# Optimization experiments

Measured on AMD Instinct MI355X. Metric: run time of the kernel, lower is better.

Reference implementation:

```python
import jax, jax.numpy as jnp
import numpy as np

# dims
T, N, F, B = 8, 100000, 128, 4096        # snapshots, graph nodes, in_features, seed batch
S1, S2 = 5, 2                             # sampling fanouts (sizes=[5,2])
H1, H2, O, C = 512, 64, 32, 2             # hids=[512,64], out_features, nchannels
TIME_MOD = 2
W_POS, W_NOPOS = 0.6, 0.4
V_TH = 1.0                                # invth=1


@jax.custom_vjp
def spike(v):
    # IF/LIF firing with threshold V_TH (spikingjelly-style heaviside)
    return (v >= V_TH).astype(v.dtype)

def _spike_fwd(v):
    return spike(v), v

def _spike_bwd(v, g):
    # triangle surrogate gradient, alpha=1.0
    return (g * jnp.maximum(0.0, 1.0 - jnp.abs(v - V_TH)),)

spike.defvjp(_spike_fwd, _spike_bwd)


def sinusoid_table(n_pos, d):
    # vectorized port of get_sinusoid_encoding_table
    pos = np.arange(n_pos, dtype=np.float32)[:, None]
    i = np.arange(d)[None, :]
    angle = pos / (10000.0 ** (2.0 * (i // 2) / d))
    tab = np.where(i % 2 == 0, np.sin(angle), np.cos(angle)).astype(np.float32)
    return jnp.asarray(tab)


def srga_single(h0, h1, h2, Ws1, Wn1, Ws2, Wn2):
    """2-layer sampled-SAGE with spiking activations (one snapshot).
    h0:[B,F] seeds, h1:[B*S1,F] hop1, h2:[B*S1*S2,F] hop2."""
    n0, n1 = h0.shape[0], h1.shape[0]
    # layer 1 applied at levels 0 and 1 (mean neighbor aggregation, no bias)
    agg0 = h1.reshape(n0, S1, -1).mean(axis=1)
    s0 = spike(h0 @ Ws1 + agg0 @ Wn1)            # [B, H1]
    agg1 = h2.reshape(n1, S2, -1).mean(axis=1)
    s1 = spike(h1 @ Ws1 + agg1 @ Wn1)            # [B*S1, H1]
    # layer 2 fuses level-1 spikes into seeds
    agg = s1.reshape(n0, S1, -1).mean(axis=1)
    return spike(s0 @ Ws2 + agg @ Wn2)            # [B, H2]


def temporal_attn(seq, w, b, pos):
    # seq: [T', B, H2]; matches TemporalAttention (softmax over time)
    if pos is not None:
        seq = seq + pos[:seq.shape[0], None, :]
    scores = jnp.einsum('tbh,ho->tbo', seq, w) + b       # [T',B,1]
    wts = jax.nn.softmax(scores, axis=0)[..., 0]          # [T',B]
    return jnp.einsum('tbh,tb->bh', seq, wts)             # [B,H2]


def setup_inputs():
    key = jax.random.key(0)
    ks = jax.random.split(key, 14)
    nodes = jax.random.randint(ks[0], (B,), 0, N)
    hop1_idx = jax.random.randint(ks[1], (T, B * S1), 0, N)
    hop2_idx = jax.random.randint(ks[2], (T, B * S1 * S2), 0, N)
    x = jax.random.normal(ks[3], (T, N, F), dtype=jnp.float32)
    inp = {
        'nodes': nodes, 'hop1_idx': hop1_idx, 'hop2_idx': hop2_idx, 'x': x,
        'Wself1': jax.random.normal(ks[4], (C, F, H1), jnp.float32) / np.sqrt(F).astype(np.float32),
        'Wnbr1': jax.random.normal(ks[5], (C, F, H1), jnp.float32) / np.sqrt(F).astype(np.float32),
        'Wself2': jax.random.normal(ks[6], (C, H1, H2), jnp.float32) / np.sqrt(H1).astype(np.float32),
        'Wnbr2': jax.random.normal(ks[7], (C, H1, H2), jnp.float32) / np.sqrt(H1).astype(np.float32),
        'attn_pos_w': jax.random.normal(ks[8], (C, H2, 1), jnp.float32) / np.sqrt(H2).astype(np.float32),
        'attn_pos_b': jax.random.normal(ks[9], (C, 1), jnp.float32) * 0.01,
        'attn_nopos_w': jax.random.normal(ks[10], (C, H2, 1), jnp.float32) / np.sqrt(H2).astype(np.float32),
        'attn_nopos_b': jax.random.normal(ks[11], (C, 1), jnp.float32) * 0.01,
        'mtg_w': jax.random.normal(ks[12], (H2, O), jnp.float32) / np.sqrt(H2).astype(np.float32),
        'mtg_b': jax.random.normal(ks[13], (O,), jnp.float32) * 0.01,
    }
    return inp


def reference(nodes, hop1_idx, hop2_idx, x, Wself1, Wnbr1, Wself2, Wnbr2,
              attn_pos_w, attn_pos_b, attn_nopos_w, attn_nopos_b, mtg_w, mtg_b):
    tidx = jnp.arange(T)
    # irregular gathers per snapshot (the memory-bound hot path)
    h0 = x[tidx[:, None], nodes[None, :]]     # [T, B, F]
    h1 = x[tidx[:, None], hop1_idx]           # [T, B*S1, F]
    h2 = x[tidx[:, None], hop2_idx]           # [T, B*S1*S2, F]
    pos_tab = sinusoid_table(T, H2)
    channel_embs = []
    for c in range(C):
        if c == 0:
            hs = (h0, h1, h2)                 # channel 0: every step
        else:
            hs = (h0[::TIME_MOD], h1[::TIME_MOD], h2[::TIME_MOD])  # channel 1: t % time_mod == 0
        outs = jax.vmap(
            lambda a, b_, d_, c=c: srga_single(a, b_, d_, Wself1[c], Wnbr1[c], Wself2[c], Wnbr2[c])
        )(*hs)                                # [T', B, H2]
        emb_pos = temporal_attn(outs, attn_pos_w[c], attn_pos_b[c], pos_tab)
        emb_nopos = temporal_attn(outs, attn_nopos_w[c], attn_nopos_b[c], None)
        channel_embs.append(W_POS * emb_pos + W_NOPOS * emb_nopos)
    stacked = jnp.stack(channel_embs, axis=0).mean(axis=0)  # [B, H2]
    return stacked @ mtg_w + mtg_b                          # [B, O]
```

## Files before the change

### kernel.cpp

```cpp
#include <hip/hip_runtime.h>
#include <math.h>

typedef _Float16 f16;
typedef _Float16 f16x8 __attribute__((ext_vector_type(8)));
typedef float f32x4 __attribute__((ext_vector_type(4)));

#define T_ 8
#define NNODES 100000
#define F_ 128
#define B_ 4096
#define S1_ 5
#define S2_ 2
#define H1_ 512
#define H2_ 64
#define O_ 32
#define M1 (B_ + B_*S1_)
#define K1 (2*F_)
#define NZ 12

__device__ __forceinline__ float wsum64(float v) {
#pragma unroll
  for (int o = 32; o > 0; o >>= 1) v += __shfl_xor(v, o, 64);
  return v;
}

__global__ __launch_bounds__(512) void postab_kernel(float* __restrict__ postab) {
  int i = threadIdx.x;
  int p = i >> 6, d = i & 63;
  double ang = (double)p / pow(10000.0, (2.0 * (double)(d >> 1)) / 64.0);
  postab[i] = (float)((d & 1) ? cos(ang) : sin(ang));
}

__global__ __launch_bounds__(256)
void prep_w(const float* __restrict__ Ws1, const float* __restrict__ Wn1,
            f16* __restrict__ Bth, f16* __restrict__ Btl) {
  const int bid = blockIdx.x;
  const int c = bid >> 9, n = bid & 511;
  const int k = threadIdx.x;
  float wv = (k < F_) ? Ws1[((size_t)c * F_ + k) * H1_ + n]
                      : Wn1[((size_t)c * F_ + (k - F_)) * H1_ + n];
  f16 hi = (f16)wv;
  f16 lo = (f16)((wv - (float)hi) * 2048.0f);
  size_t o = ((size_t)c * H1_ + n) * K1 + k;
  Bth[o] = hi; Btl[o] = lo;
}

__global__ __launch_bounds__(256)
void prep_w2(const float* __restrict__ Ws2, const float* __restrict__ Wn2,
             f16* __restrict__ B2h, f16* __restrict__ B2l) {
  const int c = blockIdx.x >> 6, n = blockIdx.x & 63;
#pragma unroll
  for (int q = 0; q < 4; ++q) {
    const int k = q * 256 + threadIdx.x;
    float v = (k < H1_) ? Ws2[((size_t)c * H1_ + k) * H2_ + n]
                        : 0.2f * Wn2[((size_t)c * H1_ + (k - H1_)) * H2_ + n];
    f16 hi = (f16)v;
    f16 lo = (f16)((v - (float)hi) * 2048.0f);
    size_t o = ((size_t)c * H2_ + n) * 1024 + k;
    B2h[o] = hi; B2l[o] = lo;
  }
}

__global__ __launch_bounds__(256) void gather_kernel(
    const int* __restrict__ nodes, const int* __restrict__ hop1,
    const int* __restrict__ hop2, const float* __restrict__ x,
    f16* __restrict__ Ah, f16* __restrict__ Al)
{
  const int t = blockIdx.y;
  const int r = blockIdx.x * 4 + (threadIdx.x >> 6);
  const int lane = threadIdx.x & 63;
  const int fo = (lane & 31) << 2;
  const bool hpart = lane < 32;
  const float* xt = x + (size_t)t * NNODES * F_;
  float4 v;
  if (r < B_) {
    if (hpart) {
      v = *(const float4*)(xt + (size_t)nodes[r] * F_ + fo);
    } else {
      v = make_float4(0.f, 0.f, 0.f, 0.f);
#pragma unroll
      for (int s = 0; s < S1_; ++s) {
        int idx = hop1[t * (B_ * S1_) + r * S1_ + s];
        float4 u = *(const float4*)(xt + (size_t)idx * F_ + fo);
        v.x += u.x; v.y += u.y; v.z += u.z; v.w += u.w;
      }
      v.x /= 5.0f; v.y /= 5.0f; v.z /= 5.0f; v.w /= 5.0f;
    }
  } else {
    const int j = r - B_;
    if (hpart) {
      v = *(const float4*)(xt + (size_t)hop1[t * (B_ * S1_) + j] * F_ + fo);
    } else {
      v = make_float4(0.f, 0.f, 0.f, 0.f);
#pragma unroll
      for (int s = 0; s < S2_; ++s) {
        int idx = hop2[t * (B_ * S1_ * S2_) + j * S2_ + s];
        float4 u = *(const float4*)(xt + (size_t)idx * F_ + fo);
        v.x += u.x; v.y += u.y; v.z += u.z; v.w += u.w;
      }
      v.x *= 0.5f; v.y *= 0.5f; v.z *= 0.5f; v.w *= 0.5f;
    }
  }
  union { f16 h[4]; uint2 u; } H, L;
  float vv[4] = {v.x, v.y, v.z, v.w};
#pragma unroll
  for (int e = 0; e < 4; ++e) {
    f16 hi = (f16)vv[e];
    H.h[e] = hi;
    L.h[e] = (f16)((vv[e] - (float)hi) * 2048.0f);
  }
  const size_t base = ((size_t)t * M1 + r) * K1 + 4 * lane;
  *(uint2*)(Ah + base) = H.u;
  *(uint2*)(Al + base) = L.u;
}

__global__ __launch_bounds__(512)
void gemm1_mfma(const f16* __restrict__ Ah, const f16* __restrict__ Al,
                const f16* __restrict__ Bth, const f16* __restrict__ Btl,
                unsigned char* __restrict__ Sbase)
{
  const int hid = blockIdx.x + 4 * blockIdx.y + 384 * blockIdx.z;
  const int xcd = hid & 7, ii = hid >> 3;
  const int nblk = ii & 3;
  const int pair = xcd * 144 + (ii >> 2);
  const int yblk = pair % 96;
  const int z    = pair / 96;

  const int t = (z < 8) ? z : 2 * (z - 8);
  const int c = (z < 8) ? 0 : 1;
  const int m0 = yblk * 256;
  const int n0 = nblk * 128;
  const int tid = threadIdx.x;
  const int lane = tid & 63;
  const int w = tid >> 6;
  const int wr = w >> 1, wc = w & 1;

  __shared__ f16 lds[3][24576];

  const f16* tbAh = Ah  + (size_t)t * M1 * K1;
  const f16* tbAl = Al  + (size_t)t * M1 * K1;
  const f16* tbBh = Bth + (size_t)c * H1_ * K1;
  const f16* tbBl = Btl + (size_t)c * H1_ * K1;

  const f16* srcp[6];
#pragma unroll
  for (int q = 0; q < 6; ++q) {
    const int u = q * 512 + tid;
    const f16* base; int row, grow;
    if (u < 1024)      { base = tbAh; row = u >> 2;          grow = m0 + row; }
    else if (u < 2048) { base = tbAl; row = (u - 1024) >> 2; grow = m0 + row; }
    else if (u < 2560) { base = tbBh; row = (u - 2048) >> 2; grow = n0 + row; }
    else               { base = tbBl; row = (u - 2560) >> 2; grow = n0 + row; }
    const int kc = (u & 3) ^ (row & 3);
    srcp[q] = base + (size_t)grow * K1 + kc * 8;
  }

  auto stage = [&](int buf) {
#pragma unroll
    for (int q = 0; q < 6; ++q) {
      __builtin_amdgcn_global_load_lds(
          (const __attribute__((address_space(1))) void*)srcp[q],
          (__attribute__((address_space(3))) void*)((char*)lds + buf * 49152 + (q * 8 + w) * 1024),
          16, 0, 0);
      srcp[q] += 32;
    }
  };

  f32x4 accm[4][4], accc[4][4];
#pragma unroll
  for (int i = 0; i < 4; ++i)
#pragma unroll
    for (int j = 0; j < 4; ++j) {
      accm[i][j] = (f32x4){0.f, 0.f, 0.f, 0.f};
      accc[i][j] = (f32x4){0.f, 0.f, 0.f, 0.f};
    }

  const int kg = lane >> 4;
  const int lr = lane & 15;
  const int ks = (kg ^ (lr & 3)) * 8;

  stage(0);
  stage(1);
  __syncthreads();

#pragma unroll
  for (int kt = 0; kt < 8; ++kt) {
    const int cur = kt % 3;
    const f16* bufp = &lds[cur][0];

    f16x8 ah[4], bh[4];
#pragma unroll
    for (int i = 0; i < 4; ++i) ah[i] = *(const f16x8*)(bufp + (wr * 64 + i * 16 + lr) * 32 + ks);
#pragma unroll
    for (int j = 0; j < 4; ++j) bh[j] = *(const f16x8*)(bufp + 16384 + (wc * 64 + j * 16 + lr) * 32 + ks);
    if (kt < 6) stage((kt + 2) % 3);
    __builtin_amdgcn_s_setprio(1);
#pragma unroll
    for (int j = 0; j < 4; ++j)
#pragma unroll
      for (int i = 0; i < 4; ++i)
        accm[i][j] = __builtin_amdgcn_mfma_f32_16x16x32_f16(ah[i], bh[j], accm[i][j], 0, 0, 0);
    __builtin_amdgcn_s_setprio(0);

    f16x8 bl[4];
#pragma unroll
    for (int j = 0; j < 4; ++j) bl[j] = *(const f16x8*)(bufp + 20480 + (wc * 64 + j * 16 + lr) * 32 + ks);
    __builtin_amdgcn_s_setprio(1);
#pragma unroll
    for (int j = 0; j < 4; ++j)
#pragma unroll
      for (int i = 0; i < 4; ++i)
        accc[i][j] = __builtin_amdgcn_mfma_f32_16x16x32_f16(ah[i], bl[j], accc[i][j], 0, 0, 0);
    __builtin_amdgcn_s_setprio(0);

    f16x8 al[4];
#pragma unroll
    for (int i = 0; i < 4; ++i) al[i] = *(const f16x8*)(bufp + 8192 + (wr * 64 + i * 16 + lr) * 32 + ks);
    __builtin_amdgcn_s_setprio(1);
#pragma unroll
    for (int j = 0; j < 4; ++j)
#pragma unroll
      for (int i = 0; i < 4; ++i)
        accc[i][j] = __builtin_amdgcn_mfma_f32_16x16x32_f16(al[i], bh[j], accc[i][j], 0, 0, 0);
    __builtin_amdgcn_s_setprio(0);

    if (kt == 1 || kt == 3 || kt == 5) {
      __syncthreads();
    } else if (kt == 0 || kt == 2 || kt == 4) {
      asm volatile("s_waitcnt lgkmcnt(0)" ::: "memory");
      __builtin_amdgcn_s_barrier();
      __builtin_amdgcn_sched_barrier(0);
    }
  }

  unsigned char* S = Sbase + (size_t)z * M1 * H1_;
#pragma unroll
  for (int i = 0; i < 4; ++i)
#pragma unroll
    for (int j = 0; j < 4; ++j) {
      const int n = n0 + wc * 64 + j * 16 + lr;
#pragma unroll
      for (int r = 0; r < 4; ++r) {
        const int m = m0 + wr * 64 + i * 16 + kg * 4 + r;
        float v = accm[i][j][r] + accc[i][j][r] * 4.8828125e-4f;
        S[(size_t)m * H1_ + n] = (v >= 1.0f) ? 1 : 0;
      }
    }
}

__global__ __launch_bounds__(256)
void gemm2_fused(const unsigned char* __restrict__ Sbase,
                 const f16* __restrict__ B2h, const f16* __restrict__ B2l,
                 unsigned char* __restrict__ outsbase)
{
  const int z = blockIdx.y;
  const int c = (z < 8) ? 0 : 1;
  const int m0 = blockIdx.x * 128;
  const int tid = threadIdx.x;
  const int lane = tid & 63;
  const int wv = tid >> 6;

  __shared__ f16 lds2[2][8192];

  const unsigned char* Sz = Sbase + (size_t)z * M1 * H1_;
  const f16* Bhc = B2h + (size_t)c * H2_ * 1024;
  const f16* Blc = B2l + (size_t)c * H2_ * 1024;

  const f16* srcB[2];
#pragma unroll
  for (int q = 0; q < 2; ++q) {
    const int v = q * 256 + tid;
    if (v < 256) {
      const int k8 = v >> 6, row = v & 63;
      srcB[q] = Bhc + (size_t)row * 1024 + k8 * 8;
    } else {
      const int v2 = v - 256, k8 = v2 >> 6, row = v2 & 63;
      srcB[q] = Blc + (size_t)row * 1024 + k8 * 8;
    }
  }
  auto stageB = [&](int buf) {
#pragma unroll
    for (int q = 0; q < 2; ++q) {
      __builtin_amdgcn_global_load_lds(
          (const __attribute__((address_space(1))) void*)srcB[q],
          (__attribute__((address_space(3))) void*)((char*)lds2 + buf * 16384 + 8192 + q * 4096 + wv * 1024),
          16, 0, 0);
      srcB[q] += 32;
    }
  };

  const int arow = tid >> 1;
  const int ahalf = tid & 1;
  const int k8b = ahalf * 2;

  auto loadS = [&](int kt, uint4* regs) {
    if (kt < 16) {
      regs[0] = *(const uint4*)(Sz + (size_t)(m0 + arow) * H1_ + kt * 32 + ahalf * 16);
    } else {
      const int k0 = (kt - 16) * 32 + ahalf * 16;
#pragma unroll
      for (int s = 0; s < S1_; ++s)
        regs[s] = *(const uint4*)(Sz + ((size_t)B_ + (size_t)(m0 + arow) * S1_ + s) * H1_ + k0);
    }
  };
  auto writeA = [&](int buf, int kt, const uint4* regs) {
    uint4 b;
    if (kt < 16) {
      b = regs[0];
    } else {
      b.x = regs[0].x + regs[1].x + regs[2].x + regs[3].x + regs[4].x;
      b.y = regs[0].y + regs[1].y + regs[2].y + regs[3].y + regs[4].y;
      b.z = regs[0].z + regs[1].z + regs[2].z + regs[3].z + regs[4].z;
      b.w = regs[0].w + regs[1].w + regs[2].w + regs[3].w + regs[4].w;
    }
    union { uint4 v; unsigned char by[16]; } U; U.v = b;
    union { f16 h[8]; uint4 v; } P0, P1;
#pragma unroll
    for (int e = 0; e < 8; ++e) {
      P0.h[e] = (f16)(int)U.by[e];
      P1.h[e] = (f16)(int)U.by[8 + e];
    }
    f16* dst = &lds2[buf][0];
    *(uint4*)(dst + ((size_t)k8b * 128 + arow) * 8)       = P0.v;
    *(uint4*)(dst + ((size_t)(k8b + 1) * 128 + arow) * 8) = P1.v;
  };

  f32x4 acch[2][4], accl[2][4];
#pragma unroll
  for (int i = 0; i < 2; ++i)
#pragma unroll
    for (int j = 0; j < 4; ++j) {
      acch[i][j] = (f32x4){0.f, 0.f, 0.f, 0.f};
      accl[i][j] = (f32x4){0.f, 0.f, 0.f, 0.f};
    }

  const int kg = lane >> 4;
  const int lr = lane & 15;

  {
    uint4 regs[5];
    loadS(0, regs);
    stageB(0);
    writeA(0, 0, regs);
  }
  __syncthreads();

#pragma unroll 1
  for (int kt = 0; kt < 32; ++kt) {
    const int cur = kt & 1;
    uint4 regs[5];
    if (kt < 31) {
      stageB(cur ^ 1);
      loadS(kt + 1, regs);
    }

    f16x8 a[2];
#pragma unroll
    for (int i = 0; i < 2; ++i)
      a[i] = *(const f16x8*)&lds2[cur][(size_t)(kg * 128 + wv * 32 + i * 16 + lr) * 8];
#pragma unroll
    for (int j = 0; j < 4; ++j) {
      f16x8 bh = *(const f16x8*)&lds2[cur][4096 + (size_t)(kg * 64 + j * 16 + lr) * 8];
      f16x8 bl = *(const f16x8*)&lds2[cur][6144 + (size_t)(kg * 64 + j * 16 + lr) * 8];
#pragma unroll
      for (int i = 0; i < 2; ++i) {
        acch[i][j] = __builtin_amdgcn_mfma_f32_16x16x32_f16(a[i], bh, acch[i][j], 0, 0, 0);
        accl[i][j] = __builtin_amdgcn_mfma_f32_16x16x32_f16(a[i], bl, accl[i][j], 0, 0, 0);
      }
    }
    if (kt < 31) writeA(cur ^ 1, kt + 1, regs);
    __syncthreads();
  }

  unsigned char* outs = outsbase + (size_t)z * B_ * H2_;
#pragma unroll
  for (int i = 0; i < 2; ++i)
#pragma unroll
    for (int j = 0; j < 4; ++j) {
      const int n = j * 16 + lr;
#pragma unroll
      for (int r = 0; r < 4; ++r) {
        const int m = m0 + wv * 32 + i * 16 + kg * 4 + r;
        float v = acch[i][j][r] + accl[i][j][r] * 4.8828125e-4f;
        outs[(size_t)m * H2_ + n] = (v >= 1.0f) ? 1 : 0;
      }
    }
}

__global__ __launch_bounds__(256)
void final_kernel(const unsigned char* __restrict__ outsbase,
                  const float* __restrict__ postab,
                  const float* __restrict__ apw, const float* __restrict__ apb,
                  const float* __restrict__ anw, const float* __restrict__ anb,
                  const float* __restrict__ mtgw, const float* __restrict__ mtgb,
                  float* __restrict__ out)
{
  const int b = blockIdx.x * 4 + (threadIdx.x >> 6);
  const int lane = threadIdx.x & 63;
  float stacked = 0.f;
#pragma unroll
  for (int c = 0; c < 2; ++c) {
    const int Tc = c ? 4 : 8;
    const int zb = c ? 8 : 0;
    const float wp = apw[c * H2_ + lane];
    const float wn = anw[c * H2_ + lane];
    float seqv[8], sp[8], sn[8];
#pragma unroll
    for (int tt = 0; tt < Tc; ++tt) {
      const float sv = (float)outsbase[((size_t)(zb + tt) * B_ + b) * H2_ + lane];
      seqv[tt] = sv;
      sp[tt] = wsum64((sv + postab[tt * H2_ + lane]) * wp);
      sn[tt] = wsum64(sv * wn);
    }
    const float bp = apb[c], bn = anb[c];
    float mp = -3.4e38f, mn = -3.4e38f;
#pragma unroll
    for (int tt = 0; tt < Tc; ++tt) {
      sp[tt] += bp; sn[tt] += bn;
      mp = fmaxf(mp, sp[tt]); mn = fmaxf(mn, sn[tt]);
    }
    float ep[8], en[8], sump = 0.f, sumn = 0.f;
#pragma unroll
    for (int tt = 0; tt < Tc; ++tt) {
      ep[tt] = expf(sp[tt] - mp);
      en[tt] = expf(sn[tt] - mn);
      sump += ep[tt]; sumn += en[tt];
    }
    float embp = 0.f, embn = 0.f;
#pragma unroll
    for (int tt = 0; tt < Tc; ++tt) {
      embp += (seqv[tt] + postab[tt * H2_ + lane]) * (ep[tt] / sump);
      embn += seqv[tt] * (en[tt] / sumn);
    }
    stacked += 0.5f * (0.6f * embp + 0.4f * embn);
  }
  float res = 0.f;
#pragma unroll
  for (int o = 0; o < O_; ++o) {
    float r = wsum64(stacked * mtgw[lane * O_ + o]);
    if (lane == o) res = r;
  }
  if (lane < O_) out[(size_t)b * O_ + lane] = res + mtgb[lane];
}

extern "C" void kernel_launch(void* const* d_in, const int* in_sizes, int n_in,
                              void* d_out, int out_size, void* d_ws, size_t ws_size,
                              hipStream_t stream)
{
  const int*   nodes  = (const int*)d_in[0];
  const int*   hop1   = (const int*)d_in[1];
  const int*   hop2   = (const int*)d_in[2];
  const float* x      = (const float*)d_in[3];
  const float* Wself1 = (const float*)d_in[4];
  const float* Wnbr1  = (const float*)d_in[5];
  const float* Wself2 = (const float*)d_in[6];
  const float* Wnbr2  = (const float*)d_in[7];
  const float* apw    = (const float*)d_in[8];
  const float* apb    = (const float*)d_in[9];
  const float* anw    = (const float*)d_in[10];
  const float* anb    = (const float*)d_in[11];
  const float* mtgw   = (const float*)d_in[12];
  const float* mtgb   = (const float*)d_in[13];
  float* out = (float*)d_out;

  char* ws = (char*)d_ws;
  size_t off = 0;
  float* postab = (float*)(ws + off);               off += 4096;
  f16* Ahb = (f16*)(ws + off);                      off += (size_t)T_ * M1 * K1 * 2;
  f16* Alb = (f16*)(ws + off);                      off += (size_t)T_ * M1 * K1 * 2;
  unsigned char* Sbase = (unsigned char*)(ws + off); off += (size_t)NZ * M1 * H1_;
  unsigned char* outsb = (unsigned char*)(ws + off); off += (size_t)NZ * B_ * H2_;
  if (ws_size < off) return;

  f16* Bth = (f16*)outsb;
  f16* Btl = Bth + (size_t)2 * H1_ * K1;
  f16* B2h = Alb;
  f16* B2l = B2h + (size_t)2 * H2_ * 1024;

  hipLaunchKernelGGL(postab_kernel, dim3(1), dim3(512), 0, stream, postab);
  hipLaunchKernelGGL(prep_w, dim3(1024), dim3(256), 0, stream, Wself1, Wnbr1, Bth, Btl);
  hipLaunchKernelGGL(gather_kernel, dim3(M1 / 4, T_), dim3(256), 0, stream,
                     nodes, hop1, hop2, x, Ahb, Alb);
  hipLaunchKernelGGL(gemm1_mfma, dim3(4, 96, NZ), dim3(512), 0, stream,
                     Ahb, Alb, Bth, Btl, Sbase);
  hipLaunchKernelGGL(prep_w2, dim3(128), dim3(256), 0, stream, Wself2, Wnbr2, B2h, B2l);
  hipLaunchKernelGGL(gemm2_fused, dim3(B_ / 128, NZ), dim3(256), 0, stream,
                     Sbase, B2h, B2l, outsb);
  hipLaunchKernelGGL(final_kernel, dim3(B_ / 4), dim3(256), 0, stream,
                     outsb, postab, apw, apb, anw, anb, mtgw, mtgb, out);
}
```

Before: 461.3 us.

## Load GEMM1 weight fragments directly from pre-laid-out global memory into registers

The weight matrix prep now writes the hi/lo fp16 weights in an MFMA-fragment-ordered layout, so each lane can read its 8-element B fragment with one vector load. GEMM1 stops staging B tiles through LDS and instead double-buffers B fragments in registers, prefetching the next k-step during the current one. This shrinks LDS per block from 144KB to 96KB and removes B-side LDS reads. In exchange it adds register pressure and relies on L2/cache hits for weight reads repeated across the two wave columns and many blocks.

```diff
diff --git a/kernel.cpp b/kernel.cpp
--- a/kernel.cpp
+++ b/kernel.cpp
@@ -41,7 +41,9 @@
                       : Wn1[((size_t)c * F_ + (k - F_)) * H1_ + n];
   f16 hi = (f16)wv;
   f16 lo = (f16)((wv - (float)hi) * 2048.0f);
-  size_t o = ((size_t)c * H1_ + n) * K1 + k;
+  const int ntile = n >> 4, lr = n & 15;
+  const int kt = k >> 5, kg = (k >> 3) & 3, ke = k & 7;
+  size_t o = ((((size_t)c * 32 + ntile) * 8 + kt) * 64 + kg * 16 + lr) * 8 + ke;
   Bth[o] = hi; Btl[o] = lo;
 }
 
@@ -129,42 +131,46 @@
   const int t = (z < 8) ? z : 2 * (z - 8);
   const int c = (z < 8) ? 0 : 1;
   const int m0 = yblk * 256;
-  const int n0 = nblk * 128;
   const int tid = threadIdx.x;
   const int lane = tid & 63;
   const int w = tid >> 6;
   const int wr = w >> 1, wc = w & 1;
 
-  __shared__ f16 lds[3][24576];
-
-  const f16* tbAh = Ah  + (size_t)t * M1 * K1;
-  const f16* tbAl = Al  + (size_t)t * M1 * K1;
-  const f16* tbBh = Bth + (size_t)c * H1_ * K1;
-  const f16* tbBl = Btl + (size_t)c * H1_ * K1;
-
-  const f16* srcp[6];
-#pragma unroll
-  for (int q = 0; q < 6; ++q) {
+  __shared__ f16 lds[3][16384];
+
+  const f16* tbAh = Ah + (size_t)t * M1 * K1;
+  const f16* tbAl = Al + (size_t)t * M1 * K1;
+
+  const f16* srcp[4];
+#pragma unroll
+  for (int q = 0; q < 4; ++q) {
     const int u = q * 512 + tid;
-    const f16* base; int row, grow;
-    if (u < 1024)      { base = tbAh; row = u >> 2;          grow = m0 + row; }
-    else if (u < 2048) { base = tbAl; row = (u - 1024) >> 2; grow = m0 + row; }
-    else if (u < 2560) { base = tbBh; row = (u - 2048) >> 2; grow = n0 + row; }
-    else               { base = tbBl; row = (u - 2560) >> 2; grow = n0 + row; }
+    const f16* base = (u < 1024) ? tbAh : tbAl;
+    const int row = (u & 1023) >> 2;
     const int kc = (u & 3) ^ (row & 3);
-    srcp[q] = base + (size_t)grow * K1 + kc * 8;
+    srcp[q] = base + (size_t)(m0 + row) * K1 + kc * 8;
   }
 
   auto stage = [&](int buf) {
 #pragma unroll
-    for (int q = 0; q < 6; ++q) {
+    for (int q = 0; q < 4; ++q) {
       __builtin_amdgcn_global_load_lds(
           (const __attribute__((address_space(1))) void*)srcp[q],
-          (__attribute__((address_space(3))) void*)((char*)lds + buf * 49152 + (q * 8 + w) * 1024),
+          (__attribute__((address_space(3))) void*)((char*)lds + buf * 32768 + (q * 8 + w) * 1024),
           16, 0, 0);
       srcp[q] += 32;
     }
   };
+
+  const f16* pBh[4];
+  const f16* pBl[4];
+#pragma unroll
+  for (int j = 0; j < 4; ++j) {
+    const int ntile = nblk * 8 + wc * 4 + j;
+    const size_t bo = (((size_t)c * 32 + ntile) * 8) * 512 + lane * 8;
+    pBh[j] = Bth + bo;
+    pBl[j] = Btl + bo;
+  }
 
   f32x4 accm[4][4], accc[4][4];
 #pragma unroll
@@ -179,6 +185,13 @@
   const int lr = lane & 15;
   const int ks = (kg ^ (lr & 3)) * 8;
 
+  f16x8 bH[2][4], bL[2][4];
+#pragma unroll
+  for (int j = 0; j < 4; ++j) {
+    bH[0][j] = *(const f16x8*)(pBh[j]);
+    bL[0][j] = *(const f16x8*)(pBl[j]);
+  }
+
   stage(0);
   stage(1);
   __syncthreads();
@@ -186,31 +199,34 @@
 #pragma unroll
   for (int kt = 0; kt < 8; ++kt) {
     const int cur = kt % 3;
+    const int pb = kt & 1;
     const f16* bufp = &lds[cur][0];
 
-    f16x8 ah[4], bh[4];
+    f16x8 ah[4];
 #pragma unroll
     for (int i = 0; i < 4; ++i) ah[i] = *(const f16x8*)(bufp + (wr * 64 + i * 16 + lr) * 32 + ks);
-#pragma unroll
-    for (int j = 0; j < 4; ++j) bh[j] = *(const f16x8*)(bufp + 16384 + (wc * 64 + j * 16 + lr) * 32 + ks);
     if (kt < 6) stage((kt + 2) % 3);
+    if (kt < 7) {
+#pragma unroll
+      for (int j = 0; j < 4; ++j) {
+        bH[pb ^ 1][j] = *(const f16x8*)(pBh[j] + (kt + 1) * 512);
+        bL[pb ^ 1][j] = *(const f16x8*)(pBl[j] + (kt + 1) * 512);
+      }
+    }
     __builtin_amdgcn_s_setprio(1);
 #pragma unroll
     for (int j = 0; j < 4; ++j)
 #pragma unroll
       for (int i = 0; i < 4; ++i)
-        accm[i][j] = __builtin_amdgcn_mfma_f32_16x16x32_f16(ah[i], bh[j], accm[i][j], 0, 0, 0);
+        accm[i][j] = __builtin_amdgcn_mfma_f32_16x16x32_f16(ah[i], bH[pb][j], accm[i][j], 0, 0, 0);
     __builtin_amdgcn_s_setprio(0);
 
-    f16x8 bl[4];
-#pragma unroll
-    for (int j = 0; j < 4; ++j) bl[j] = *(const f16x8*)(bufp + 20480 + (wc * 64 + j * 16 + lr) * 32 + ks);
     __builtin_amdgcn_s_setprio(1);
 #pragma unroll
     for (int j = 0; j < 4; ++j)
 #pragma unroll
       for (int i = 0; i < 4; ++i)
-        accc[i][j] = __builtin_amdgcn_mfma_f32_16x16x32_f16(ah[i], bl[j], accc[i][j], 0, 0, 0);
+        accc[i][j] = __builtin_amdgcn_mfma_f32_16x16x32_f16(ah[i], bL[pb][j], accc[i][j], 0, 0, 0);
     __builtin_amdgcn_s_setprio(0);
 
     f16x8 al[4];
@@ -221,7 +237,7 @@
     for (int j = 0; j < 4; ++j)
 #pragma unroll
       for (int i = 0; i < 4; ++i)
-        accc[i][j] = __builtin_amdgcn_mfma_f32_16x16x32_f16(al[i], bh[j], accc[i][j], 0, 0, 0);
+        accc[i][j] = __builtin_amdgcn_mfma_f32_16x16x32_f16(al[i], bH[pb][j], accc[i][j], 0, 0, 0);
     __builtin_amdgcn_s_setprio(0);
 
     if (kt == 1 || kt == 3 || kt == 5) {
@@ -233,6 +249,7 @@
     }
   }
 
+  const int n0 = nblk * 128;
   unsigned char* S = Sbase + (size_t)z * M1 * H1_;
 #pragma unroll
   for (int i = 0; i < 4; ++i)
```

Result: slower. 476.1 us (+3.2%).
